# Kernel optimization log

Hardware: AMD Instinct MI355X
Metric: run time of the kernel (lower is better)

The kernel has to match this reference:

```python
import jax, jax.numpy as jnp
import numpy as np

IN_FEATURES = 1024
OUT_FEATURES = 1024
NUM_GRIDS = 8
GRID_MIN, GRID_MAX = -2.0, 2.0
DENOM = (GRID_MAX - GRID_MIN) / (NUM_GRIDS - 1)
LN_EPS = 1e-5
GRID = jnp.linspace(GRID_MIN, GRID_MAX, NUM_GRIDS)


def setup_inputs() -> dict:
    key = jax.random.key(0)
    k_x, k_sw, k_bw = jax.random.split(key, 3)
    N = 8192
    x = jax.random.normal(k_x, (N, IN_FEATURES), dtype=jnp.float32)
    ln_gamma = jnp.ones((IN_FEATURES,), dtype=jnp.float32)
    ln_beta = jnp.zeros((IN_FEATURES,), dtype=jnp.float32)
    # trunc_normal(std=0.1) approximated by scaled normal
    spline_w = 0.1 * jax.random.normal(k_sw, (OUT_FEATURES, IN_FEATURES * NUM_GRIDS), dtype=jnp.float32)
    base_w = jax.random.normal(k_bw, (OUT_FEATURES, IN_FEATURES), dtype=jnp.float32) * (1.0 / np.sqrt(IN_FEATURES))
    base_b = jnp.zeros((OUT_FEATURES,), dtype=jnp.float32)
    return {"x": x, "ln_gamma": ln_gamma, "ln_beta": ln_beta,
            "spline_w": spline_w, "base_w": base_w, "base_b": base_b}


def reference(x, ln_gamma, ln_beta, spline_w, base_w, base_b):
    # LayerNorm over last dim
    mu = jnp.mean(x, axis=-1, keepdims=True)
    var = jnp.var(x, axis=-1, keepdims=True)
    xn = (x - mu) * jax.lax.rsqrt(var + LN_EPS) * ln_gamma + ln_beta
    # RBF basis: [N, in, G]
    basis = jnp.exp(-jnp.square((xn[..., None] - GRID) / DENOM))
    basis = basis.reshape(x.shape[0], IN_FEATURES * NUM_GRIDS)
    y = jnp.einsum('nk,ok->no', basis, spline_w)
    y = y + jnp.einsum('nd,od->no', jax.nn.silu(x), base_w) + base_b
    return y
```

## Files before the change

kernel.cpp:

```cpp
#include <hip/hip_runtime.h>
#include <hip/hip_bf16.h>
#include <stdint.h>

#define IN_F 1024
#define OUT_F 1024
#define NG 8
#define KSPLINE 8192
#define KDIM 9216
#define M_ROWS 8192
#define LOG2E 1.4426950408889634f
#define DENOMV 0.5714285714285714f
#define INV_DENOM 1.75f

using bf16_t = __bf16;
using bf16x8 = __attribute__((ext_vector_type(8))) __bf16;
using f32x4  = __attribute__((ext_vector_type(4))) float;

#define AS1 __attribute__((address_space(1)))
#define AS3 __attribute__((address_space(3)))

__device__ inline unsigned short f2bf(float f) {
    unsigned int u = __float_as_uint(f);
    u += 0x7fffu + ((u >> 16) & 1u);
    return (unsigned short)(u >> 16);
}

__global__ __launch_bounds__(256) void prep_w_kernel(
        const float* __restrict__ sw, const float* __restrict__ bw,
        bf16_t* __restrict__ W) {
    int idx = blockIdx.x * 256 + threadIdx.x;
    int o   = idx / 2304;
    int k4  = idx - o * 2304;
    float4 v;
    if (k4 < 2048) v = ((const float4*)sw)[(size_t)o * 2048 + k4];
    else           v = ((const float4*)bw)[(size_t)o * 256 + (k4 - 2048)];
    unsigned int lo = (unsigned int)f2bf(v.x) | ((unsigned int)f2bf(v.y) << 16);
    unsigned int hi = (unsigned int)f2bf(v.z) | ((unsigned int)f2bf(v.w) << 16);
    ((uint2*)W)[idx] = make_uint2(lo, hi);
}

__global__ __launch_bounds__(256) void prep_a_kernel(
        const float* __restrict__ x, const float* __restrict__ gamma,
        const float* __restrict__ beta, bf16_t* __restrict__ A) {
    const int wave = threadIdx.x >> 6, lane = threadIdx.x & 63;
    const int row = blockIdx.x * 4 + wave;
    const float* xr = x + (size_t)row * IN_F;

    float xv[16];
    float s = 0.0f, s2 = 0.0f;
#pragma unroll
    for (int j = 0; j < 16; ++j) {
        float v = xr[j * 64 + lane];
        xv[j] = v;
        s += v;
        s2 += v * v;
    }
#pragma unroll
    for (int off = 32; off > 0; off >>= 1) {
        s  += __shfl_xor(s, off);
        s2 += __shfl_xor(s2, off);
    }
    float mu   = s * (1.0f / IN_F);
    float var  = s2 * (1.0f / IN_F) - mu * mu;
    float rstd = rsqrtf(var + 1e-5f);

    bf16_t* Arow = A + (size_t)row * KDIM;
    uint4* basis_out = (uint4*)Arow;
    unsigned short* silu_out = (unsigned short*)(Arow + KSPLINE);
#pragma unroll
    for (int j = 0; j < 16; ++j) {
        int f = j * 64 + lane;
        float xs = xv[j];
        float xn = (xs - mu) * rstd * gamma[f] + beta[f];
        unsigned int pk[4];
#pragma unroll
        for (int g = 0; g < 4; ++g) {
            float t0 = (xn - (-2.0f + (float)(2 * g)     * DENOMV)) * INV_DENOM;
            float t1 = (xn - (-2.0f + (float)(2 * g + 1) * DENOMV)) * INV_DENOM;
            float b0 = exp2f(t0 * t0 * -LOG2E);
            float b1 = exp2f(t1 * t1 * -LOG2E);
            pk[g] = (unsigned int)f2bf(b0) | ((unsigned int)f2bf(b1) << 16);
        }
        basis_out[f] = make_uint4(pk[0], pk[1], pk[2], pk[3]);
        float sg = xs / (1.0f + exp2f(-xs * LOG2E));
        silu_out[f] = f2bf(sg);
    }
}

__global__ __launch_bounds__(256, 2) void gemm_kernel(
        const bf16_t* __restrict__ A, const bf16_t* __restrict__ W,
        const float* __restrict__ bias, float* __restrict__ C) {
    __shared__ alignas(16) bf16_t As[128 * 32];
    __shared__ alignas(16) bf16_t Bs[128 * 32];
    const int bm = blockIdx.x, bn = blockIdx.y;
    const int tid = threadIdx.x;
    const int wave = tid >> 6, lane = tid & 63;
    const int wm = wave >> 1, wn = wave & 1;

    f32x4 acc[4][4] = {};

    const bf16_t* gAj[2];
    const bf16_t* gBj[2];
    int ldsOff[2];
#pragma unroll
    for (int j = 0; j < 2; ++j) {
        int chunk = wave * 128 + j * 64 + lane;
        int r  = chunk >> 2;
        int c8 = (chunk & 3) * 8;
        gAj[j] = A + (size_t)(bm * 128 + r) * KDIM + c8;
        gBj[j] = W + (size_t)(bn * 128 + r) * KDIM + c8;
        ldsOff[j] = chunk * 8;
    }

    const int lm = lane & 15;
    const int lk = (lane >> 4) * 8;

    for (int kt = 0; kt < KDIM / 32; ++kt) {
        __syncthreads();
#pragma unroll
        for (int j = 0; j < 2; ++j) {
            __builtin_amdgcn_global_load_lds(
                (const AS1 void*)(gAj[j] + kt * 32), (AS3 void*)(As + ldsOff[j]), 16, 0, 0);
            __builtin_amdgcn_global_load_lds(
                (const AS1 void*)(gBj[j] + kt * 32), (AS3 void*)(Bs + ldsOff[j]), 16, 0, 0);
        }
        __syncthreads();

        bf16x8 a[4], b[4];
#pragma unroll
        for (int i = 0; i < 4; ++i) {
            a[i] = *(const bf16x8*)(As + (wm * 64 + i * 16 + lm) * 32 + lk);
            b[i] = *(const bf16x8*)(Bs + (wn * 64 + i * 16 + lm) * 32 + lk);
        }
#pragma unroll
        for (int mi = 0; mi < 4; ++mi)
#pragma unroll
            for (int ni = 0; ni < 4; ++ni)
                acc[mi][ni] = __builtin_amdgcn_mfma_f32_16x16x32_bf16(
                    a[mi], b[ni], acc[mi][ni], 0, 0, 0);
    }

    const int cn = lane & 15;
    const int rm = (lane >> 4) * 4;
#pragma unroll
    for (int ni = 0; ni < 4; ++ni) {
        int col = bn * 128 + wn * 64 + ni * 16 + cn;
        float bv = bias[col];
#pragma unroll
        for (int mi = 0; mi < 4; ++mi) {
            int row = bm * 128 + wm * 64 + mi * 16 + rm;
            float* Cp = C + (size_t)row * OUT_F + col;
#pragma unroll
            for (int r = 0; r < 4; ++r)
                Cp[(size_t)r * OUT_F] = acc[mi][ni][r] + bv;
        }
    }
}

extern "C" void kernel_launch(void* const* d_in, const int* in_sizes, int n_in,
                              void* d_out, int out_size, void* d_ws, size_t ws_size,
                              hipStream_t stream) {
    const float* x     = (const float*)d_in[0];
    const float* gamma = (const float*)d_in[1];
    const float* beta  = (const float*)d_in[2];
    const float* sw    = (const float*)d_in[3];
    const float* bw    = (const float*)d_in[4];
    const float* bb    = (const float*)d_in[5];
    float* out = (float*)d_out;

    char* ws = (char*)d_ws;
    const size_t Wbytes = (size_t)OUT_F * KDIM * 2;
    bf16_t* Wb = (bf16_t*)ws;
    bf16_t* Ab = (bf16_t*)(ws + Wbytes);

    const size_t rowBytes = (size_t)KDIM * 2;
    size_t avail = ws_size > Wbytes ? ws_size - Wbytes : 0;
    int chunk = (int)(avail / rowBytes);
    chunk &= ~127;
    if (chunk > M_ROWS) chunk = M_ROWS;
    if (chunk < 128) chunk = 128;

    prep_w_kernel<<<(OUT_F * 2304) / 256, 256, 0, stream>>>(sw, bw, Wb);

    for (int r0 = 0; r0 < M_ROWS; r0 += chunk) {
        int rows = (M_ROWS - r0) < chunk ? (M_ROWS - r0) : chunk;
        prep_a_kernel<<<rows / 4, 256, 0, stream>>>(x + (size_t)r0 * IN_F, gamma, beta, Ab);
        dim3 g(rows / 128, OUT_F / 128);
        gemm_kernel<<<g, dim3(256), 0, stream>>>(Ab, Wb, bb, out + (size_t)r0 * OUT_F);
    }
}
```

Measured before the change: 334.6 us.

## Generate RBF basis on the fly inside the GEMM instead of materializing it

Instead of writing a full 8192x9216 basis matrix to memory, the prep kernel now stores only the scaled, transposed normalized input and SiLU values in fp16. The GEMM computes the eight Gaussian basis values per input feature in registers from one scalar load and feeds them directly to MFMA. This removes the large A-matrix write and reread and the row-chunking loop. The cost is extra exp2 work inside the GEMM inner loop, plus fp16 precision in place of bf16.

```diff
diff --git a/kernel.cpp b/kernel.cpp
--- a/kernel.cpp
+++ b/kernel.cpp
@@ -9,41 +9,36 @@
 #define KDIM 9216
 #define M_ROWS 8192
 #define LOG2E 1.4426950408889634f
-#define DENOMV 0.5714285714285714f
-#define INV_DENOM 1.75f
-
-using bf16_t = __bf16;
-using bf16x8 = __attribute__((ext_vector_type(8))) __bf16;
+#define KC 2.1019642153762872f
+
+using half4v = __attribute__((ext_vector_type(4))) _Float16;
+using half8  = __attribute__((ext_vector_type(8))) _Float16;
 using f32x4  = __attribute__((ext_vector_type(4))) float;
 
 #define AS1 __attribute__((address_space(1)))
 #define AS3 __attribute__((address_space(3)))
 
-__device__ inline unsigned short f2bf(float f) {
-    unsigned int u = __float_as_uint(f);
-    u += 0x7fffu + ((u >> 16) & 1u);
-    return (unsigned short)(u >> 16);
-}
-
 __global__ __launch_bounds__(256) void prep_w_kernel(
         const float* __restrict__ sw, const float* __restrict__ bw,
-        bf16_t* __restrict__ W) {
+        _Float16* __restrict__ W) {
     int idx = blockIdx.x * 256 + threadIdx.x;
     int o   = idx / 2304;
     int k4  = idx - o * 2304;
     float4 v;
     if (k4 < 2048) v = ((const float4*)sw)[(size_t)o * 2048 + k4];
     else           v = ((const float4*)bw)[(size_t)o * 256 + (k4 - 2048)];
-    unsigned int lo = (unsigned int)f2bf(v.x) | ((unsigned int)f2bf(v.y) << 16);
-    unsigned int hi = (unsigned int)f2bf(v.z) | ((unsigned int)f2bf(v.w) << 16);
-    ((uint2*)W)[idx] = make_uint2(lo, hi);
-}
-
-__global__ __launch_bounds__(256) void prep_a_kernel(
+    half4v h = { (_Float16)v.x, (_Float16)v.y, (_Float16)v.z, (_Float16)v.w };
+    *(half4v*)(W + (size_t)idx * 4) = h;
+}
+
+__global__ __launch_bounds__(1024) void prep_ln_kernel(
         const float* __restrict__ x, const float* __restrict__ gamma,
-        const float* __restrict__ beta, bf16_t* __restrict__ A) {
-    const int wave = threadIdx.x >> 6, lane = threadIdx.x & 63;
-    const int row = blockIdx.x * 4 + wave;
+        const float* __restrict__ beta, _Float16* __restrict__ xqT,
+        _Float16* __restrict__ silu) {
+    __shared__ float lds[512 * 20];
+    const int w = threadIdx.x >> 6, lane = threadIdx.x & 63;
+    const int rowbase = blockIdx.x * 16;
+    const int row = rowbase + w;
     const float* xr = x + (size_t)row * IN_F;
 
     float xv[16];
@@ -64,34 +59,42 @@
     float var  = s2 * (1.0f / IN_F) - mu * mu;
     float rstd = rsqrtf(var + 1e-5f);
 
-    bf16_t* Arow = A + (size_t)row * KDIM;
-    uint4* basis_out = (uint4*)Arow;
-    unsigned short* silu_out = (unsigned short*)(Arow + KSPLINE);
+    _Float16* srow = silu + (size_t)row * IN_F;
 #pragma unroll
     for (int j = 0; j < 16; ++j) {
         int f = j * 64 + lane;
         float xs = xv[j];
-        float xn = (xs - mu) * rstd * gamma[f] + beta[f];
-        unsigned int pk[4];
-#pragma unroll
-        for (int g = 0; g < 4; ++g) {
-            float t0 = (xn - (-2.0f + (float)(2 * g)     * DENOMV)) * INV_DENOM;
-            float t1 = (xn - (-2.0f + (float)(2 * g + 1) * DENOMV)) * INV_DENOM;
-            float b0 = exp2f(t0 * t0 * -LOG2E);
-            float b1 = exp2f(t1 * t1 * -LOG2E);
-            pk[g] = (unsigned int)f2bf(b0) | ((unsigned int)f2bf(b1) << 16);
-        }
-        basis_out[f] = make_uint4(pk[0], pk[1], pk[2], pk[3]);
-        float sg = xs / (1.0f + exp2f(-xs * LOG2E));
-        silu_out[f] = f2bf(sg);
-    }
-}
-
-__global__ __launch_bounds__(256, 2) void gemm_kernel(
-        const bf16_t* __restrict__ A, const bf16_t* __restrict__ W,
-        const float* __restrict__ bias, float* __restrict__ C) {
-    __shared__ alignas(16) bf16_t As[128 * 32];
-    __shared__ alignas(16) bf16_t Bs[128 * 32];
+        srow[f] = (_Float16)(xs / (1.0f + exp2f(-xs * LOG2E)));
+    }
+
+#pragma unroll
+    for (int p = 0; p < 2; ++p) {
+        __syncthreads();
+#pragma unroll
+        for (int j2 = 0; j2 < 8; ++j2) {
+            int j = p * 8 + j2;
+            int f = j * 64 + lane;
+            float xn = (xv[j] - mu) * rstd * gamma[f] + beta[f];
+            lds[(j2 * 64 + lane) * 20 + w] = xn * KC;
+        }
+        __syncthreads();
+        int t  = threadIdx.x;
+        int fl = t >> 1;
+        int rh = (t & 1) * 8;
+        float4 v0 = *(const float4*)(lds + fl * 20 + rh);
+        float4 v1 = *(const float4*)(lds + fl * 20 + rh + 4);
+        half8 h = { (_Float16)v0.x, (_Float16)v0.y, (_Float16)v0.z, (_Float16)v0.w,
+                    (_Float16)v1.x, (_Float16)v1.y, (_Float16)v1.z, (_Float16)v1.w };
+        *(half8*)(xqT + (size_t)(p * 512 + fl) * M_ROWS + rowbase + rh) = h;
+    }
+}
+
+__global__ __launch_bounds__(256, 2) void gemm_fused_kernel(
+        const _Float16* __restrict__ xqT, const _Float16* __restrict__ silu,
+        const _Float16* __restrict__ W, const float* __restrict__ bias,
+        float* __restrict__ C) {
+    __shared__ alignas(16) _Float16 As[128 * 32];
+    __shared__ alignas(16) _Float16 Bs[128 * 32];
     const int bm = blockIdx.x, bn = blockIdx.y;
     const int tid = threadIdx.x;
     const int wave = tid >> 6, lane = tid & 63;
@@ -99,44 +102,89 @@
 
     f32x4 acc[4][4] = {};
 
-    const bf16_t* gAj[2];
-    const bf16_t* gBj[2];
+    const _Float16* gB[2];
+    const _Float16* gAb[2];
     int ldsOff[2];
 #pragma unroll
     for (int j = 0; j < 2; ++j) {
         int chunk = wave * 128 + j * 64 + lane;
         int r  = chunk >> 2;
         int c8 = (chunk & 3) * 8;
-        gAj[j] = A + (size_t)(bm * 128 + r) * KDIM + c8;
-        gBj[j] = W + (size_t)(bn * 128 + r) * KDIM + c8;
+        gB[j]  = W    + (size_t)(bn * 128 + r) * KDIM + c8;
+        gAb[j] = silu + (size_t)(bm * 128 + r) * IN_F + c8;
         ldsOff[j] = chunk * 8;
     }
 
     const int lm = lane & 15;
     const int lk = (lane >> 4) * 8;
 
-    for (int kt = 0; kt < KDIM / 32; ++kt) {
+    const float cq[8] = {
+        -2.0000000f * KC, -1.4285715f * KC, -0.8571429f * KC, -0.2857143f * KC,
+         0.2857143f * KC,  0.8571429f * KC,  1.4285715f * KC,  2.0000000f * KC };
+
+    const _Float16* xqp = xqT + (size_t)(lane >> 4) * M_ROWS
+                              + (size_t)bm * 128 + wm * 64 + lm;
+
+    for (int kt = 0; kt < KSPLINE / 32; ++kt) {
+        __syncthreads();
+#pragma unroll
+        for (int j = 0; j < 2; ++j)
+            __builtin_amdgcn_global_load_lds(
+                (const AS1 void*)(gB[j] + kt * 32), (AS3 void*)(Bs + ldsOff[j]), 16, 0, 0);
+        float xqv[4];
+#pragma unroll
+        for (int mi = 0; mi < 4; ++mi)
+            xqv[mi] = (float)xqp[(size_t)kt * 4 * M_ROWS + mi * 16];
+        __syncthreads();
+
+        half8 b[4];
+#pragma unroll
+        for (int i = 0; i < 4; ++i)
+            b[i] = *(const half8*)(Bs + (wn * 64 + i * 16 + lm) * 32 + lk);
+
+        half8 a[4];
+#pragma unroll
+        for (int mi = 0; mi < 4; ++mi) {
+            float q = xqv[mi];
+            half8 h;
+#pragma unroll
+            for (int g = 0; g < 8; ++g) {
+                float v = q - cq[g];
+                h[g] = (_Float16)exp2f(-(v * v));
+            }
+            a[mi] = h;
+        }
+
+#pragma unroll
+        for (int mi = 0; mi < 4; ++mi)
+#pragma unroll
+            for (int ni = 0; ni < 4; ++ni)
+                acc[mi][ni] = __builtin_amdgcn_mfma_f32_16x16x32_f16(
+                    a[mi], b[ni], acc[mi][ni], 0, 0, 0);
+    }
+
+    for (int kt = 0; kt < IN_F / 32; ++kt) {
         __syncthreads();
 #pragma unroll
         for (int j = 0; j < 2; ++j) {
             __builtin_amdgcn_global_load_lds(
-                (const AS1 void*)(gAj[j] + kt * 32), (AS3 void*)(As + ldsOff[j]), 16, 0, 0);
+                (const AS1 void*)(gAb[j] + kt * 32), (AS3 void*)(As + ldsOff[j]), 16, 0, 0);
             __builtin_amdgcn_global_load_lds(
-                (const AS1 void*)(gBj[j] + kt * 32), (AS3 void*)(Bs + ldsOff[j]), 16, 0, 0);
-        }
-        __syncthreads();
-
-        bf16x8 a[4], b[4];
+                (const AS1 void*)(gB[j] + KSPLINE + kt * 32), (AS3 void*)(Bs + ldsOff[j]), 16, 0, 0);
+        }
+        __syncthreads();
+
+        half8 a[4], b[4];
 #pragma unroll
         for (int i = 0; i < 4; ++i) {
-            a[i] = *(const bf16x8*)(As + (wm * 64 + i * 16 + lm) * 32 + lk);
-            b[i] = *(const bf16x8*)(Bs + (wn * 64 + i * 16 + lm) * 32 + lk);
+            a[i] = *(const half8*)(As + (wm * 64 + i * 16 + lm) * 32 + lk);
+            b[i] = *(const half8*)(Bs + (wn * 64 + i * 16 + lm) * 32 + lk);
         }
 #pragma unroll
         for (int mi = 0; mi < 4; ++mi)
 #pragma unroll
             for (int ni = 0; ni < 4; ++ni)
-                acc[mi][ni] = __builtin_amdgcn_mfma_f32_16x16x32_bf16(
+                acc[mi][ni] = __builtin_amdgcn_mfma_f32_16x16x32_f16(
                     a[mi], b[ni], acc[mi][ni], 0, 0, 0);
     }
 
@@ -169,23 +217,13 @@
     float* out = (float*)d_out;
 
     char* ws = (char*)d_ws;
-    const size_t Wbytes = (size_t)OUT_F * KDIM * 2;
-    bf16_t* Wb = (bf16_t*)ws;
-    bf16_t* Ab = (bf16_t*)(ws + Wbytes);
-
-    const size_t rowBytes = (size_t)KDIM * 2;
-    size_t avail = ws_size > Wbytes ? ws_size - Wbytes : 0;
-    int chunk = (int)(avail / rowBytes);
-    chunk &= ~127;
-    if (chunk > M_ROWS) chunk = M_ROWS;
-    if (chunk < 128) chunk = 128;
+    _Float16* Wb   = (_Float16*)ws;
+    _Float16* xqT  = (_Float16*)(ws + (size_t)OUT_F * KDIM * 2);
+    _Float16* silu = (_Float16*)(ws + (size_t)OUT_F * KDIM * 2
+                                    + (size_t)IN_F * M_ROWS * 2);
 
     prep_w_kernel<<<(OUT_F * 2304) / 256, 256, 0, stream>>>(sw, bw, Wb);
-
-    for (int r0 = 0; r0 < M_ROWS; r0 += chunk) {
-        int rows = (M_ROWS - r0) < chunk ? (M_ROWS - r0) : chunk;
-        prep_a_kernel<<<rows / 4, 256, 0, stream>>>(x + (size_t)r0 * IN_F, gamma, beta, Ab);
-        dim3 g(rows / 128, OUT_F / 128);
-        gemm_kernel<<<g, dim3(256), 0, stream>>>(Ab, Wb, bb, out + (size_t)r0 * OUT_F);
-    }
-}
+    prep_ln_kernel<<<M_ROWS / 16, 1024, 0, stream>>>(x, gamma, beta, xqT, silu);
+    gemm_fused_kernel<<<dim3(M_ROWS / 128, OUT_F / 128), 256, 0, stream>>>(
+        xqT, silu, Wb, bb, out);
+}
```

Result: slower. 523.9 us (+56.6%).

## Switch GEMM operands to fp16, merge prep kernels, simplify RBF math

Applied to the files above, without the earlier changes.

Converts the basis, SiLU and weight operands from bf16 to fp16, using hardware conversion and the f16 MFMA instead of manual bf16 rounding. The weight and activation prep kernels become one launch with a block-index split, and the RBF exponent is folded into a single constant so each basis value is one subtract, one square and one exp2. The workspace-chunking loop is removed, so the full A matrix is assumed to fit in the workspace. fp16 has a narrower range than bf16, which is fine for the bounded basis and weights, but the unchunked layout could overrun a smaller workspace.

```diff
diff --git a/kernel.cpp b/kernel.cpp
--- a/kernel.cpp
+++ b/kernel.cpp
@@ -9,39 +9,34 @@
 #define KDIM 9216
 #define M_ROWS 8192
 #define LOG2E 1.4426950408889634f
-#define DENOMV 0.5714285714285714f
-#define INV_DENOM 1.75f
+#define KC 2.1019642153762872f
 
-using bf16_t = __bf16;
-using bf16x8 = __attribute__((ext_vector_type(8))) __bf16;
+#define A_BLOCKS (M_ROWS / 4)
+#define W_BLOCKS ((OUT_F * 2304) / 256)
+
+using half4v = __attribute__((ext_vector_type(4))) _Float16;
+using half8  = __attribute__((ext_vector_type(8))) _Float16;
 using f32x4  = __attribute__((ext_vector_type(4))) float;
 
 #define AS1 __attribute__((address_space(1)))
 #define AS3 __attribute__((address_space(3)))
 
-__device__ inline unsigned short f2bf(float f) {
-    unsigned int u = __float_as_uint(f);
-    u += 0x7fffu + ((u >> 16) & 1u);
-    return (unsigned short)(u >> 16);
-}
-
-__global__ __launch_bounds__(256) void prep_w_kernel(
-        const float* __restrict__ sw, const float* __restrict__ bw,
-        bf16_t* __restrict__ W) {
-    int idx = blockIdx.x * 256 + threadIdx.x;
-    int o   = idx / 2304;
-    int k4  = idx - o * 2304;
-    float4 v;
-    if (k4 < 2048) v = ((const float4*)sw)[(size_t)o * 2048 + k4];
-    else           v = ((const float4*)bw)[(size_t)o * 256 + (k4 - 2048)];
-    unsigned int lo = (unsigned int)f2bf(v.x) | ((unsigned int)f2bf(v.y) << 16);
-    unsigned int hi = (unsigned int)f2bf(v.z) | ((unsigned int)f2bf(v.w) << 16);
-    ((uint2*)W)[idx] = make_uint2(lo, hi);
-}
-
-__global__ __launch_bounds__(256) void prep_a_kernel(
+__global__ __launch_bounds__(256) void prep_kernel(
         const float* __restrict__ x, const float* __restrict__ gamma,
-        const float* __restrict__ beta, bf16_t* __restrict__ A) {
+        const float* __restrict__ beta, const float* __restrict__ sw,
+        const float* __restrict__ bw, _Float16* __restrict__ A,
+        _Float16* __restrict__ W) {
+    if (blockIdx.x >= A_BLOCKS) {
+        int idx = (blockIdx.x - A_BLOCKS) * 256 + threadIdx.x;
+        int o   = idx / 2304;
+        int k4  = idx - o * 2304;
+        float4 v;
+        if (k4 < 2048) v = ((const float4*)sw)[(size_t)o * 2048 + k4];
+        else           v = ((const float4*)bw)[(size_t)o * 256 + (k4 - 2048)];
+        half4v h = { (_Float16)v.x, (_Float16)v.y, (_Float16)v.z, (_Float16)v.w };
+        *(half4v*)(W + (size_t)idx * 4) = h;
+        return;
+    }
     const int wave = threadIdx.x >> 6, lane = threadIdx.x & 63;
     const int row = blockIdx.x * 4 + wave;
     const float* xr = x + (size_t)row * IN_F;
@@ -64,34 +59,34 @@
     float var  = s2 * (1.0f / IN_F) - mu * mu;
     float rstd = rsqrtf(var + 1e-5f);
 
-    bf16_t* Arow = A + (size_t)row * KDIM;
-    uint4* basis_out = (uint4*)Arow;
-    unsigned short* silu_out = (unsigned short*)(Arow + KSPLINE);
+    const float cq[8] = {
+        -2.0000000f * KC, -1.4285715f * KC, -0.8571429f * KC, -0.2857143f * KC,
+         0.2857143f * KC,  0.8571429f * KC,  1.4285715f * KC,  2.0000000f * KC };
+
+    _Float16* Arow = A + (size_t)row * KDIM;
+    half8* basis_out = (half8*)Arow;
+    _Float16* silu_out = Arow + KSPLINE;
 #pragma unroll
     for (int j = 0; j < 16; ++j) {
         int f = j * 64 + lane;
         float xs = xv[j];
-        float xn = (xs - mu) * rstd * gamma[f] + beta[f];
-        unsigned int pk[4];
+        float xq = ((xs - mu) * rstd * gamma[f] + beta[f]) * KC;
+        half8 h;
 #pragma unroll
-        for (int g = 0; g < 4; ++g) {
-            float t0 = (xn - (-2.0f + (float)(2 * g)     * DENOMV)) * INV_DENOM;
-            float t1 = (xn - (-2.0f + (float)(2 * g + 1) * DENOMV)) * INV_DENOM;
-            float b0 = exp2f(t0 * t0 * -LOG2E);
-            float b1 = exp2f(t1 * t1 * -LOG2E);
-            pk[g] = (unsigned int)f2bf(b0) | ((unsigned int)f2bf(b1) << 16);
+        for (int g = 0; g < 8; ++g) {
+            float v = xq - cq[g];
+            h[g] = (_Float16)exp2f(-(v * v));
         }
-        basis_out[f] = make_uint4(pk[0], pk[1], pk[2], pk[3]);
-        float sg = xs / (1.0f + exp2f(-xs * LOG2E));
-        silu_out[f] = f2bf(sg);
+        basis_out[f] = h;
+        silu_out[f] = (_Float16)(xs / (1.0f + exp2f(-xs * LOG2E)));
     }
 }
 
 __global__ __launch_bounds__(256, 2) void gemm_kernel(
-        const bf16_t* __restrict__ A, const bf16_t* __restrict__ W,
+        const _Float16* __restrict__ A, const _Float16* __restrict__ W,
         const float* __restrict__ bias, float* __restrict__ C) {
-    __shared__ alignas(16) bf16_t As[128 * 32];
-    __shared__ alignas(16) bf16_t Bs[128 * 32];
+    __shared__ alignas(16) _Float16 As[128 * 32];
+    __shared__ alignas(16) _Float16 Bs[128 * 32];
     const int bm = blockIdx.x, bn = blockIdx.y;
     const int tid = threadIdx.x;
     const int wave = tid >> 6, lane = tid & 63;
@@ -99,8 +94,8 @@
 
     f32x4 acc[4][4] = {};
 
-    const bf16_t* gAj[2];
-    const bf16_t* gBj[2];
+    const _Float16* gAj[2];
+    const _Float16* gBj[2];
     int ldsOff[2];
 #pragma unroll
     for (int j = 0; j < 2; ++j) {
@@ -126,17 +121,17 @@
         }
         __syncthreads();
 
-        bf16x8 a[4], b[4];
+        half8 a[4], b[4];
 #pragma unroll
         for (int i = 0; i < 4; ++i) {
-            a[i] = *(const bf16x8*)(As + (wm * 64 + i * 16 + lm) * 32 + lk);
-            b[i] = *(const bf16x8*)(Bs + (wn * 64 + i * 16 + lm) * 32 + lk);
+            a[i] = *(const half8*)(As + (wm * 64 + i * 16 + lm) * 32 + lk);
+            b[i] = *(const half8*)(Bs + (wn * 64 + i * 16 + lm) * 32 + lk);
         }
 #pragma unroll
         for (int mi = 0; mi < 4; ++mi)
 #pragma unroll
             for (int ni = 0; ni < 4; ++ni)
-                acc[mi][ni] = __builtin_amdgcn_mfma_f32_16x16x32_bf16(
+                acc[mi][ni] = __builtin_amdgcn_mfma_f32_16x16x32_f16(
                     a[mi], b[ni], acc[mi][ni], 0, 0, 0);
     }
 
@@ -169,23 +164,11 @@
     float* out = (float*)d_out;
 
     char* ws = (char*)d_ws;
-    const size_t Wbytes = (size_t)OUT_F * KDIM * 2;
-    bf16_t* Wb = (bf16_t*)ws;
-    bf16_t* Ab = (bf16_t*)(ws + Wbytes);
+    _Float16* Wb = (_Float16*)ws;
+    _Float16* Ab = (_Float16*)(ws + (size_t)OUT_F * KDIM * 2);
 
-    const size_t rowBytes = (size_t)KDIM * 2;
-    size_t avail = ws_size > Wbytes ? ws_size - Wbytes : 0;
-    int chunk = (int)(avail / rowBytes);
-    chunk &= ~127;
-    if (chunk > M_ROWS) chunk = M_ROWS;
-    if (chunk < 128) chunk = 128;
-
-    prep_w_kernel<<<(OUT_F * 2304) / 256, 256, 0, stream>>>(sw, bw, Wb);
-
-    for (int r0 = 0; r0 < M_ROWS; r0 += chunk) {
-        int rows = (M_ROWS - r0) < chunk ? (M_ROWS - r0) : chunk;
-        prep_a_kernel<<<rows / 4, 256, 0, stream>>>(x + (size_t)r0 * IN_F, gamma, beta, Ab);
-        dim3 g(rows / 128, OUT_F / 128);
-        gemm_kernel<<<g, dim3(256), 0, stream>>>(Ab, Wb, bb, out + (size_t)r0 * OUT_F);
-    }
+    prep_kernel<<<A_BLOCKS + W_BLOCKS, 256, 0, stream>>>(
+        x, gamma, beta, sw, bw, Ab, Wb);
+    gemm_kernel<<<dim3(M_ROWS / 128, OUT_F / 128), 256, 0, stream>>>(
+        Ab, Wb, bb, out);
 }
```

Measured after the change: 324.9 us. -2.9%, faster.
